# Performance work log

Measured on AMD Instinct MI355X. Metric: run time of the kernel, lower is better.

## Reference

```python
import jax, jax.numpy as jnp
import numpy as np

N_GRAPHS = 256
EPS = 1e-5


def _bn(x, g, b):
    # training-mode BatchNorm1d: biased batch statistics
    m = jnp.mean(x, axis=0)
    v = jnp.mean((x - m) ** 2, axis=0)
    return (x - m) * jax.lax.rsqrt(v + EPS) * g + b


def _gcn_conv(x, W, b, src, dst, dinv, n_nodes):
    # GCNConv: D^{-1/2} (A + I) D^{-1/2} X W + b
    h = x @ W  # [N, H]
    coef = dinv[src] * dinv[dst]  # [E]
    msg = h[src] * coef[:, None]  # [E, H]
    agg = jax.ops.segment_sum(msg, dst, num_segments=n_nodes)
    agg = agg + h * (dinv * dinv)[:, None]  # self-loop term
    return agg + b


def setup_inputs() -> dict:
    key = jax.random.key(0)
    ks = jax.random.split(key, 20)
    N, E, D, H, C = 50000, 600000, 128, 128, 10
    L = 3  # num_conv_layers
    x = jax.random.normal(ks[0], (N, D), dtype=jnp.float32)
    edge_index = jax.random.randint(ks[1], (2, E), 0, N, dtype=jnp.int64)
    batch = jnp.sort(jax.random.randint(ks[2], (N,), 0, N_GRAPHS, dtype=jnp.int64))

    def xavier(k, shape):
        fan_in, fan_out = shape[0], shape[1]
        lim = float(np.sqrt(6.0 / (fan_in + fan_out)))
        return jax.random.uniform(k, shape, jnp.float32, -lim, lim)

    return {
        "x": x,
        "edge_index": edge_index,
        "batch": batch,
        "bn_feat_g": jnp.ones((D,), jnp.float32),
        "bn_feat_b": jnp.full((D,), 1e-4, jnp.float32),
        "conv_feat_W": xavier(ks[3], (D, H)),
        "conv_feat_b": jnp.zeros((H,), jnp.float32),
        "conv_W": jnp.stack([xavier(ks[4 + i], (H, H)) for i in range(L)]),
        "conv_b": jnp.zeros((L, H), jnp.float32),
        "bn_conv_g": jnp.ones((L, H), jnp.float32),
        "bn_conv_b": jnp.full((L, H), 1e-4, jnp.float32),
        "gate_W1": xavier(ks[8], (H, H)),
        "gate_b1": jnp.zeros((H,), jnp.float32),
        "gate_W2": xavier(ks[9], (H, 1)),
        "gate_b2": jnp.zeros((1,), jnp.float32),
        "fc_W": xavier(ks[10], (H, H)),
        "fc_b": jnp.zeros((H,), jnp.float32),
        "bn_fc_g": jnp.ones((H,), jnp.float32),
        "bn_fc_b": jnp.full((H,), 1e-4, jnp.float32),
        "cls_W": xavier(ks[11], (H, C)),
        "cls_b": jnp.zeros((C,), jnp.float32),
    }


def reference(x, edge_index, batch, bn_feat_g, bn_feat_b, conv_feat_W, conv_feat_b,
              conv_W, conv_b, bn_conv_g, bn_conv_b, gate_W1, gate_b1, gate_W2,
              gate_b2, fc_W, fc_b, bn_fc_g, bn_fc_b, cls_W, cls_b):
    N = x.shape[0]
    src, dst = edge_index[0], edge_index[1]
    # degree incl. self-loop (edge weights = 1)
    deg = jax.ops.segment_sum(jnp.ones_like(src, dtype=x.dtype), dst, num_segments=N) + 1.0
    dinv = jax.lax.rsqrt(deg)

    h = _bn(x, bn_feat_g, bn_feat_b)
    h = jax.nn.relu(_gcn_conv(h, conv_feat_W, conv_feat_b, src, dst, dinv, N))
    for i in range(conv_W.shape[0]):
        h = jax.nn.relu(_gcn_conv(_bn(h, bn_conv_g[i], bn_conv_b[i]),
                                  conv_W[i], conv_b[i], src, dst, dinv, N))
    gate = jax.nn.sigmoid(jax.nn.relu(h @ gate_W1 + gate_b1) @ gate_W2 + gate_b2)  # [N,1]
    g = jax.ops.segment_sum(h * gate, batch, num_segments=N_GRAPHS)  # [G, H]
    g = jax.nn.relu(_bn(g, bn_fc_g, bn_fc_b) @ fc_W + fc_b)
    logits = g @ cls_W + cls_b
    return jax.nn.log_softmax(logits, axis=-1)
```

## Files before the change

### kernel.cpp

```cpp
#include <hip/hip_runtime.h>
#include <hip/hip_fp16.h>

typedef unsigned short u16;
typedef unsigned int u32;
typedef __attribute__((ext_vector_type(8))) short short8;
typedef __attribute__((ext_vector_type(4))) float floatx4;

#define EPSI 1e-5f

__device__ __forceinline__ float b2f(u16 h) { return __uint_as_float(((u32)h) << 16); }
__device__ __forceinline__ u16 f2b(float f) {
    u32 u = __float_as_uint(f);
    return (u16)((u + 0x7fffu + ((u >> 16) & 1u)) >> 16);
}
__device__ __forceinline__ u32 pack2(float a, float b) {
    return (u32)f2b(a) | ((u32)f2b(b) << 16);
}
__device__ __forceinline__ float ldf(const void* p, int i, int fm) {
    if (fm == 1) return b2f(((const u16*)p)[i]);
    if (fm == 2) return __half2float(__ushort_as_half(((const u16*)p)[i]));
    return ((const float*)p)[i];
}
__device__ __forceinline__ int ldi(const void* p, int i, int im) {
    return im ? ((const int*)p)[2 * i] : ((const int*)p)[i];
}

__device__ __forceinline__ void acc8(float* a, int4 v, float w) {
    u32 x = (u32)v.x, y = (u32)v.y, z = (u32)v.z, q = (u32)v.w;
    a[0] += b2f((u16)x) * w;
    a[1] += b2f((u16)(x >> 16)) * w;
    a[2] += b2f((u16)y) * w;
    a[3] += b2f((u16)(y >> 16)) * w;
    a[4] += b2f((u16)z) * w;
    a[5] += b2f((u16)(z >> 16)) * w;
    a[6] += b2f((u16)q) * w;
    a[7] += b2f((u16)(q >> 16)) * w;
}

__global__ void init_kernel(u32* zp, int nz, const void* ones, const void* ei, int* flags) {
    int i = blockIdx.x * 256 + threadIdx.x;
    if (i < nz) zp[i] = 0;
    if (blockIdx.x == 0 && threadIdx.x == 0) {
        u32 w = ((const u32*)ones)[0];
        int fm = 0;
        if (w == 0x3F803F80u) fm = 1;
        else if (w == 0x3C003C00u) fm = 2;
        const u32* e = (const u32*)ei;
        int all0 = 1;
        for (int k = 0; k < 16; ++k)
            if (e[2 * k + 1] != 0u) all0 = 0;
        flags[0] = fm;
        flags[1] = all0;
    }
}

__global__ void bigprep_kernel(const void* __restrict__ ei, int* __restrict__ cnt, int E,
                               const void* __restrict__ batch, int* __restrict__ bounds, int N,
                               int EB, const void* __restrict__ x, u32* __restrict__ A2,
                               float* __restrict__ stats0, const void* __restrict__ gW1,
                               const void* __restrict__ gb1, u16* __restrict__ Wtg,
                               float* __restrict__ bias2g, const void* __restrict__ cfW,
                               const void* __restrict__ cW, u16* __restrict__ Wt4,
                               const void* __restrict__ fcW, float* __restrict__ fcWf,
                               const void* __restrict__ clsW, float* __restrict__ clsWf,
                               const void* __restrict__ fcb, float* __restrict__ fcbf,
                               const void* __restrict__ clsb, float* __restrict__ clsbf,
                               const void* __restrict__ gW2, float* __restrict__ gW2f,
                               const void* __restrict__ gb2, float* __restrict__ gb2f,
                               const void* __restrict__ cfb, const void* __restrict__ cvb,
                               float* __restrict__ biasf, const int* __restrict__ flags) {
    int fm = flags[0];
    int bid = blockIdx.x, t = threadIdx.x;
    if (bid < EB) {
        int im = flags[1];
        int g = bid * 256 + t;
        if (g < E) atomicAdd(&cnt[ldi(ei, E + g, im)], 1);
        if (g < N) {
            int b = ldi(batch, g, im);
            if (g == 0) {
                for (int q = 0; q <= b; ++q) bounds[q] = 0;
            } else {
                int bp = ldi(batch, g - 1, im);
                for (int q = bp + 1; q <= b; ++q) bounds[q] = g;
            }
            if (g == N - 1) {
                for (int q = b + 1; q <= 256; ++q) bounds[q] = N;
            }
        }
        return;
    }
    int pid = bid - EB;
    if (pid < 1024) {
        int np = N * 64;
        float s0 = 0.f, s1 = 0.f, q0 = 0.f, q1 = 0.f;
        if (fm == 1) {
            const u32* xs = (const u32*)x;
            for (int j = pid * 256 + t; j < np; j += 1024 * 256) {
                u32 w = xs[j];
                A2[j] = w;
                float v0 = b2f((u16)w), v1 = b2f((u16)(w >> 16));
                s0 += v0;
                q0 += v0 * v0;
                s1 += v1;
                q1 += v1 * v1;
            }
        } else {
            for (int j = pid * 256 + t; j < np; j += 1024 * 256) {
                float v0 = ldf(x, 2 * j, fm);
                float v1 = ldf(x, 2 * j + 1, fm);
                A2[j] = pack2(v0, v1);
                s0 += v0;
                q0 += v0 * v0;
                s1 += v1;
                q1 += v1 * v1;
            }
        }
        __shared__ float2 sh[256];
        sh[t] = make_float2(s0, s1);
        __syncthreads();
        float* so = stats0 + (pid & 15) * 256;
        if (t < 64) {
            float a = 0.f, b = 0.f;
#pragma unroll
            for (int w = 0; w < 4; ++w) {
                float2 v = sh[t + w * 64];
                a += v.x;
                b += v.y;
            }
            atomicAdd(&so[2 * t], a);
            atomicAdd(&so[2 * t + 1], b);
        }
        __syncthreads();
        sh[t] = make_float2(q0, q1);
        __syncthreads();
        if (t < 64) {
            float a = 0.f, b = 0.f;
#pragma unroll
            for (int w = 0; w < 4; ++w) {
                float2 v = sh[t + w * 64];
                a += v.x;
                b += v.y;
            }
            atomicAdd(&so[128 + 2 * t], a);
            atomicAdd(&so[128 + 2 * t + 1], b);
        }
    } else if (pid < 1152) {
        int n = pid - 1024;
        if (t < 128) Wtg[n * 128 + t] = f2b(ldf(gW1, t * 128 + n, fm));
        if (t == 0) bias2g[n] = ldf(gb1, n, fm);
    } else if (pid < 1216) {
        int task = pid - 1152;
        int mat = task >> 4, tile = task & 15;
        int tr = (tile >> 2) * 32, tc = (tile & 3) * 32;
        const void* src = mat == 0 ? cfW : cW;
        int soff = mat == 0 ? 0 : (mat - 1) * 16384;
        __shared__ float tb[32][33];
#pragma unroll
        for (int i = 0; i < 4; ++i) {
            int o = t * 4 + i;
            int r = o >> 5, c = o & 31;
            tb[r][c] = ldf(src, soff + (tr + r) * 128 + tc + c, fm);
        }
        __syncthreads();
        u16* dst = Wt4 + mat * 16384;
#pragma unroll
        for (int i = 0; i < 4; ++i) {
            int o = t * 4 + i;
            int nr = o >> 5, kc = o & 31;
            dst[(tc + nr) * 128 + tr + kc] = f2b(tb[kc][nr]);
        }
    } else if (pid < 1224) {
        int base = (pid - 1216) * 2048;
        for (int i = t; i < 2048; i += 256) fcWf[base + i] = ldf(fcW, base + i, fm);
    } else {
        for (int i = t; i < 1280; i += 256) clsWf[i] = ldf(clsW, i, fm);
        for (int i = t; i < 512; i += 256)
            biasf[i] = (i < 128) ? ldf(cfb, i, fm) : ldf(cvb, i - 128, fm);
        if (t < 128) {
            fcbf[t] = ldf(fcb, t, fm);
            gW2f[t] = ldf(gW2, t, fm);
        }
        if (t < 10) clsbf[t] = ldf(clsb, t, fm);
        if (t == 0) gb2f[0] = ldf(gb2, 0, fm);
    }
}

__global__ void scan_kernel(const int* __restrict__ cnt, int* __restrict__ row_start, int n) {
    int b = blockIdx.x, t = threadIdx.x;
    __shared__ int sh[256];
    const int4* c4 = (const int4*)cnt;
    int lim4 = b * 256;
    int acc = 0;
    for (int i = t; i < lim4; i += 256) {
        int4 v = c4[i];
        acc += v.x + v.y + v.z + v.w;
    }
    sh[t] = acc;
    __syncthreads();
    for (int o = 128; o > 0; o >>= 1) {
        if (t < o) sh[t] += sh[t + o];
        __syncthreads();
    }
    int pre = sh[0];
    __syncthreads();
    int base = b * 1024 + t * 4;
    int v[4];
    int s = 0;
#pragma unroll
    for (int j = 0; j < 4; ++j) {
        int idx = base + j;
        v[j] = (idx < n) ? cnt[idx] : 0;
        s += v[j];
    }
    sh[t] = s;
    __syncthreads();
    for (int o = 1; o < 256; o <<= 1) {
        int add = (t >= o) ? sh[t - o] : 0;
        __syncthreads();
        sh[t] += add;
        __syncthreads();
    }
    int run = pre + sh[t] - s;
#pragma unroll
    for (int j = 0; j < 4; ++j) {
        int idx = base + j;
        run += v[j];
        if (idx < n) row_start[idx + 1] = run;
    }
    if (b == 0 && t == 0) row_start[0] = 0;
}

__global__ __launch_bounds__(256) void mfma_fill_kernel(
    const u16* __restrict__ A, const u16* __restrict__ Wt, const float* __restrict__ stats,
    const void* __restrict__ bng, const void* __restrict__ bnb, u16* __restrict__ C, int N,
    int mmgrid, const void* __restrict__ ei, const int* __restrict__ row_start,
    int* __restrict__ fill_cnt, const int* __restrict__ cnt, int2* __restrict__ edges, int E,
    const int* __restrict__ flags) {
    int t = threadIdx.x;
    if ((int)blockIdx.x >= mmgrid) {
        int im = flags[1];
        int e = (blockIdx.x - mmgrid) * 256 + t;
        if (e < E) {
            int s = ldi(ei, e, im);
            int d = ldi(ei, E + e, im);
            int p = row_start[d] + atomicAdd(&fill_cnt[d], 1);
            float cf = rsqrtf((float)cnt[s] + 1.0f) * rsqrtf((float)cnt[d] + 1.0f);
            edges[p] = make_int2(s, __float_as_int(cf));
        }
        return;
    }
    int fm = flags[0];
    __shared__ float scs[128], shs[128];
    if (t < 128) {
        float ms = 0.f, qs = 0.f;
#pragma unroll
        for (int c = 0; c < 16; ++c) {
            ms += stats[c * 256 + t];
            qs += stats[c * 256 + 128 + t];
        }
        float m = ms / (float)N;
        float var = qs / (float)N - m * m;
        float rs = rsqrtf(var + EPSI);
        float sc = rs * ldf(bng, t, fm);
        scs[t] = sc;
        shs[t] = ldf(bnb, t, fm) - m * sc;
    }
    __syncthreads();
    int wid = t >> 6, lane = t & 63;
    int m16 = lane & 15, q = lane >> 4;
    int row0 = blockIdx.x * 64 + wid * 16;
    if (row0 >= N) return;
    int arow = row0 + m16;
    floatx4 acc[8];
#pragma unroll
    for (int i = 0; i < 8; ++i) acc[i] = (floatx4){0.f, 0.f, 0.f, 0.f};
#pragma unroll
    for (int kc = 0; kc < 4; ++kc) {
        short8 af;
        if (arow < N) {
            short8 raw = *(const short8*)&A[(size_t)arow * 128 + kc * 32 + q * 8];
            int k0 = kc * 32 + q * 8;
#pragma unroll
            for (int j = 0; j < 8; ++j)
                af[j] = (short)f2b(b2f((u16)raw[j]) * scs[k0 + j] + shs[k0 + j]);
        } else {
#pragma unroll
            for (int j = 0; j < 8; ++j) af[j] = 0;
        }
#pragma unroll
        for (int nt = 0; nt < 8; ++nt) {
            short8 bf = *(const short8*)&Wt[(nt * 16 + m16) * 128 + kc * 32 + q * 8];
            acc[nt] = __builtin_amdgcn_mfma_f32_16x16x32_bf16(af, bf, acc[nt], 0, 0, 0);
        }
    }
#pragma unroll
    for (int nt = 0; nt < 8; ++nt) {
#pragma unroll
        for (int reg = 0; reg < 4; ++reg) {
            int r = row0 + q * 4 + reg;
            if (r < N) C[(size_t)r * 128 + nt * 16 + m16] = f2b(acc[nt][reg]);
        }
    }
}

__global__ __launch_bounds__(256) void mfma_mm_kernel(
    const u16* __restrict__ A, const u16* __restrict__ Wt, const float* __restrict__ stats,
    const void* __restrict__ bng, const void* __restrict__ bnb, int poff,
    const float* __restrict__ bias2, u16* __restrict__ C, float* __restrict__ gate,
    const float* __restrict__ gW2f, const float* __restrict__ gb2f, int N, int mode,
    const int* __restrict__ flags) {
    int t = threadIdx.x;
    __shared__ float scs[128], shs[128];
    if (stats && t < 128) {
        int fm = flags[0];
        float ms = 0.f, qs = 0.f;
#pragma unroll
        for (int c = 0; c < 16; ++c) {
            ms += stats[c * 256 + t];
            qs += stats[c * 256 + 128 + t];
        }
        float m = ms / (float)N;
        float var = qs / (float)N - m * m;
        float rs = rsqrtf(var + EPSI);
        float sc = rs * ldf(bng, poff + t, fm);
        scs[t] = sc;
        shs[t] = ldf(bnb, poff + t, fm) - m * sc;
    }
    __syncthreads();
    int wid = t >> 6, lane = t & 63;
    int m16 = lane & 15, q = lane >> 4;
    int row0 = blockIdx.x * 64 + wid * 16;
    if (row0 >= N) return;
    int arow = row0 + m16;
    floatx4 acc[8];
#pragma unroll
    for (int i = 0; i < 8; ++i) acc[i] = (floatx4){0.f, 0.f, 0.f, 0.f};
#pragma unroll
    for (int kc = 0; kc < 4; ++kc) {
        short8 af;
        if (arow < N) {
            if (stats) {
                short8 raw = *(const short8*)&A[(size_t)arow * 128 + kc * 32 + q * 8];
                int k0 = kc * 32 + q * 8;
#pragma unroll
                for (int j = 0; j < 8; ++j)
                    af[j] = (short)f2b(b2f((u16)raw[j]) * scs[k0 + j] + shs[k0 + j]);
            } else {
                af = *(const short8*)&A[(size_t)arow * 128 + kc * 32 + q * 8];
            }
        } else {
#pragma unroll
            for (int j = 0; j < 8; ++j) af[j] = 0;
        }
#pragma unroll
        for (int nt = 0; nt < 8; ++nt) {
            short8 bf = *(const short8*)&Wt[(nt * 16 + m16) * 128 + kc * 32 + q * 8];
            acc[nt] = __builtin_amdgcn_mfma_f32_16x16x32_bf16(af, bf, acc[nt], 0, 0, 0);
        }
    }
    if (mode == 0) {
#pragma unroll
        for (int nt = 0; nt < 8; ++nt) {
#pragma unroll
            for (int reg = 0; reg < 4; ++reg) {
                int r = row0 + q * 4 + reg;
                if (r < N) C[(size_t)r * 128 + nt * 16 + m16] = f2b(acc[nt][reg]);
            }
        }
    } else {
        float p[4] = {0.f, 0.f, 0.f, 0.f};
#pragma unroll
        for (int nt = 0; nt < 8; ++nt) {
            float b2v = bias2[nt * 16 + m16];
            float w2v = gW2f[nt * 16 + m16];
#pragma unroll
            for (int reg = 0; reg < 4; ++reg)
                p[reg] += fmaxf(acc[nt][reg] + b2v, 0.0f) * w2v;
        }
        float gb = gb2f[0];
#pragma unroll
        for (int reg = 0; reg < 4; ++reg) {
            float v = p[reg];
            v += __shfl_xor(v, 1);
            v += __shfl_xor(v, 2);
            v += __shfl_xor(v, 4);
            v += __shfl_xor(v, 8);
            if (m16 == 0) {
                int r = row0 + q * 4 + reg;
                if (r < N) gate[r] = 1.0f / (1.0f + expf(-(v + gb)));
            }
        }
    }
}

__global__ __launch_bounds__(512) void agg_kernel(
    const u32* __restrict__ C2, const int* __restrict__ row_start,
    const int2* __restrict__ edges, const float* __restrict__ biasf, int boff,
    u32* __restrict__ A2, float* __restrict__ statsOut, int N) {
    int t = threadIdx.x;
    int wid = t >> 6, lane = t & 63;
    int g = lane >> 4, p = lane & 15;
    int n = blockIdx.x * 8 + wid;
    float acc[8];
#pragma unroll
    for (int j = 0; j < 8; ++j) acc[j] = 0.f;
    if (n < N) {
        int rs = row_start[n], re = row_start[n + 1];
        if (g == 0) {
            float d2 = 1.0f / ((float)(re - rs) + 1.0f);
            int4 s = *(const int4*)&C2[(size_t)n * 64 + p * 4];
            acc8(acc, s, d2);
        }
        for (int e = rs; e < re; e += 16) {
            int iA = e + g, iB = e + 4 + g, iC = e + 8 + g, iD = e + 12 + g;
            int2 eA = edges[iA < re ? iA : re - 1];
            int2 eB = edges[iB < re ? iB : re - 1];
            int2 eC = edges[iC < re ? iC : re - 1];
            int2 eD = edges[iD < re ? iD : re - 1];
            int4 vA = *(const int4*)&C2[(size_t)eA.x * 64 + p * 4];
            int4 vB = *(const int4*)&C2[(size_t)eB.x * 64 + p * 4];
            int4 vC = *(const int4*)&C2[(size_t)eC.x * 64 + p * 4];
            int4 vD = *(const int4*)&C2[(size_t)eD.x * 64 + p * 4];
            acc8(acc, vA, iA < re ? __int_as_float(eA.y) : 0.f);
            acc8(acc, vB, iB < re ? __int_as_float(eB.y) : 0.f);
            acc8(acc, vC, iC < re ? __int_as_float(eC.y) : 0.f);
            acc8(acc, vD, iD < re ? __int_as_float(eD.y) : 0.f);
        }
    }
#pragma unroll
    for (int j = 0; j < 8; ++j) {
        acc[j] += __shfl_xor(acc[j], 16);
        acc[j] += __shfl_xor(acc[j], 32);
    }
    __shared__ float xch[8][128];
    if (g == 0) {
#pragma unroll
        for (int j = 0; j < 8; ++j) xch[wid][p * 8 + j] = acc[j];
    }
    __syncthreads();
    float ax = 0.f, ay = 0.f;
    if (n < N) {
        float2 bv = ((const float2*)(biasf + boff))[lane];
        float2 v = ((const float2*)xch[wid])[lane];
        ax = fmaxf(v.x + bv.x, 0.0f);
        ay = fmaxf(v.y + bv.y, 0.0f);
        A2[(size_t)n * 64 + lane] = pack2(ax, ay);
    }
    if (!statsOut) return;
    __shared__ float2 sh[512];
    sh[t] = make_float2(ax, ay);
    __syncthreads();
    float* so = statsOut + (blockIdx.x & 15) * 256;
    if (t < 64) {
        float a = 0.f, b = 0.f;
#pragma unroll
        for (int w = 0; w < 8; ++w) {
            float2 v = sh[t + w * 64];
            a += v.x;
            b += v.y;
        }
        atomicAdd(&so[2 * t], a);
        atomicAdd(&so[2 * t + 1], b);
    }
    __syncthreads();
    sh[t] = make_float2(ax * ax, ay * ay);
    __syncthreads();
    if (t < 64) {
        float a = 0.f, b = 0.f;
#pragma unroll
        for (int w = 0; w < 8; ++w) {
            float2 v = sh[t + w * 64];
            a += v.x;
            b += v.y;
        }
        atomicAdd(&so[128 + 2 * t], a);
        atomicAdd(&so[128 + 2 * t + 1], b);
    }
}

__global__ void pool_kernel(const u32* __restrict__ A2, const float* __restrict__ gate,
                            const int* __restrict__ bounds, float* __restrict__ pooled,
                            float* __restrict__ statsP) {
    int g = blockIdx.x;
    int t = threadIdx.x;
    int f2 = t & 63, grp = t >> 6;
    int s = bounds[g], e = bounds[g + 1];
    float ax = 0.f, ay = 0.f;
    int r = s + grp;
    for (; r + 4 < e; r += 8) {
        u32 v0 = A2[(size_t)r * 64 + f2];
        u32 v1 = A2[(size_t)(r + 4) * 64 + f2];
        float g0 = gate[r], g1 = gate[r + 4];
        ax += b2f((u16)v0) * g0;
        ay += b2f((u16)(v0 >> 16)) * g0;
        ax += b2f((u16)v1) * g1;
        ay += b2f((u16)(v1 >> 16)) * g1;
    }
    if (r < e) {
        u32 v0 = A2[(size_t)r * 64 + f2];
        float g0 = gate[r];
        ax += b2f((u16)v0) * g0;
        ay += b2f((u16)(v0 >> 16)) * g0;
    }
    __shared__ float2 sh[256];
    sh[t] = make_float2(ax, ay);
    __syncthreads();
    if (t < 64) {
        float2 a = sh[t], b = sh[t + 64], c = sh[t + 128], d = sh[t + 192];
        float x = a.x + b.x + c.x + d.x;
        float y = a.y + b.y + c.y + d.y;
        ((float2*)(pooled + g * 128))[t] = make_float2(x, y);
        float* so = statsP + (g & 7) * 256;
        atomicAdd(&so[2 * t], x);
        atomicAdd(&so[2 * t + 1], y);
        atomicAdd(&so[128 + 2 * t], x * x);
        atomicAdd(&so[128 + 2 * t + 1], y * y);
    }
}

__global__ __launch_bounds__(256) void fc_cls_kernel(
    const float* __restrict__ pooled, const float* __restrict__ statsP,
    const void* __restrict__ bng, const void* __restrict__ bnb,
    const float* __restrict__ fcWf, const float* __restrict__ fcbf,
    const float* __restrict__ clsWf, const float* __restrict__ clsbf, void* __restrict__ out,
    const int* __restrict__ flags) {
    int fm = flags[0];
    int g = blockIdx.x, t = threadIdx.x;
    __shared__ float pv[128];
    __shared__ float red[256];
    __shared__ float fco[128];
    __shared__ float lg[10];
    __shared__ float redv[2];
    if (t < 128) {
        float ms = 0.f, qs = 0.f;
#pragma unroll
        for (int c = 0; c < 8; ++c) {
            ms += statsP[c * 256 + t];
            qs += statsP[c * 256 + 128 + t];
        }
        float m = ms / 256.0f;
        float var = qs / 256.0f - m * m;
        float rs = rsqrtf(var + EPSI);
        float sc = rs * ldf(bng, t, fm);
        pv[t] = pooled[g * 128 + t] * sc + (ldf(bnb, t, fm) - m * sc);
    }
    __syncthreads();
    {
        int j = t & 127, half = t >> 7;
        float acc = 0.f;
        int k0 = half * 64;
#pragma unroll 8
        for (int k = k0; k < k0 + 64; ++k) acc += pv[k] * fcWf[k * 128 + j];
        red[t] = acc;
    }
    __syncthreads();
    if (t < 128) fco[t] = fmaxf(red[t] + red[t + 128] + fcbf[t], 0.0f);
    __syncthreads();
    if (t < 10) {
        float a = clsbf[t];
#pragma unroll 8
        for (int k = 0; k < 128; ++k) a += fco[k] * clsWf[k * 10 + t];
        lg[t] = a;
    }
    __syncthreads();
    if (t == 0) {
        float mx = lg[0];
        for (int j = 1; j < 10; ++j) mx = fmaxf(mx, lg[j]);
        float se = 0.f;
        for (int j = 0; j < 10; ++j) se += expf(lg[j] - mx);
        redv[0] = mx;
        redv[1] = logf(se);
    }
    __syncthreads();
    if (t < 10) {
        float v = lg[t] - redv[0] - redv[1];
        if (fm == 1) ((u16*)out)[g * 10 + t] = f2b(v);
        else if (fm == 2) ((u16*)out)[g * 10 + t] = __half_as_ushort(__float2half(v));
        else ((float*)out)[g * 10 + t] = v;
    }
}

extern "C" void kernel_launch(void* const* d_in, const int* in_sizes, int n_in,
                              void* d_out, int out_size, void* d_ws, size_t ws_size,
                              hipStream_t stream) {
    const void* x = d_in[0];
    const void* ei = d_in[1];
    const void* batch = d_in[2];
    const void* bn_feat_g = d_in[3];
    const void* bn_feat_b = d_in[4];
    const void* conv_feat_W = d_in[5];
    const void* conv_feat_b = d_in[6];
    const void* conv_W = d_in[7];
    const void* conv_b = d_in[8];
    const void* bn_conv_g = d_in[9];
    const void* bn_conv_b = d_in[10];
    const void* gate_W1 = d_in[11];
    const void* gate_b1 = d_in[12];
    const void* gate_W2 = d_in[13];
    const void* gate_b2 = d_in[14];
    const void* fc_W = d_in[15];
    const void* fc_b = d_in[16];
    const void* bn_fc_g = d_in[17];
    const void* bn_fc_b = d_in[18];
    const void* cls_W = d_in[19];
    const void* cls_b = d_in[20];

    const int N = in_sizes[2];
    const int E = in_sizes[1] / 2;
    const int NB = (N + 1023) / 1024;
    const int EB = ((E > N ? E : N) + 255) / 256;

    u32* ws = (u32*)d_ws;
    size_t off = 0;
    auto alloc = [&](size_t n) {
        size_t o = off;
        off += (n + 63) & ~(size_t)63;
        return o;
    };
    size_t o_cnt = alloc(N);
    size_t o_fill = alloc(N);
    size_t o_stats = alloc(5 * 4096);
    size_t o_statsP = alloc(2048);
    size_t zero_end = off;
    size_t o_flags = alloc(16);
    size_t o_rs = alloc((size_t)N + 1);
    size_t o_edges = alloc((size_t)E * 2);
    size_t o_wtg = alloc(128 * 128 / 2);
    size_t o_b2g = alloc(128);
    size_t o_Wt4 = alloc(4 * 16384 / 2);
    size_t o_fcW = alloc(16384);
    size_t o_fcb = alloc(128);
    size_t o_clsW = alloc(1280);
    size_t o_clsb = alloc(16);
    size_t o_gW2 = alloc(128);
    size_t o_gb2 = alloc(16);
    size_t o_biasf = alloc(512);
    size_t o_gate = alloc(N);
    size_t o_bnd = alloc(257);
    size_t o_pool = alloc(256 * 128);
    size_t o_A = alloc((size_t)N * 64);
    size_t o_C = alloc((size_t)N * 64);
    (void)ws_size;
    (void)n_in;
    (void)out_size;

    int* cnt = (int*)(ws + o_cnt);
    int* fillc = (int*)(ws + o_fill);
    float* stats = (float*)(ws + o_stats);
    float* statsP = (float*)(ws + o_statsP);
    int* flags = (int*)(ws + o_flags);
    int* row_start = (int*)(ws + o_rs);
    int2* edges = (int2*)(ws + o_edges);
    u16* Wtg = (u16*)(ws + o_wtg);
    float* bias2g = (float*)(ws + o_b2g);
    u16* Wt4 = (u16*)(ws + o_Wt4);
    float* fcWf = (float*)(ws + o_fcW);
    float* fcbf = (float*)(ws + o_fcb);
    float* clsWf = (float*)(ws + o_clsW);
    float* clsbf = (float*)(ws + o_clsb);
    float* gW2f = (float*)(ws + o_gW2);
    float* gb2f = (float*)(ws + o_gb2);
    float* biasf = (float*)(ws + o_biasf);
    float* gateb = (float*)(ws + o_gate);
    int* bnd = (int*)(ws + o_bnd);
    float* pooled = (float*)(ws + o_pool);
    u16* A = (u16*)(ws + o_A);
    u16* C = (u16*)(ws + o_C);

    int nz = (int)zero_end;
    init_kernel<<<(nz + 255) / 256, 256, 0, stream>>>(ws, nz, bn_feat_g, ei, flags);
    bigprep_kernel<<<EB + 1225, 256, 0, stream>>>(
        ei, cnt, E, batch, bnd, N, EB, x, (u32*)A, stats, gate_W1, gate_b1, Wtg, bias2g,
        conv_feat_W, conv_W, Wt4, fc_W, fcWf, cls_W, clsWf, fc_b, fcbf, cls_b, clsbf, gate_W2,
        gW2f, gate_b2, gb2f, conv_feat_b, conv_b, biasf, flags);
    scan_kernel<<<NB, 256, 0, stream>>>(cnt, row_start, N);

    int mmgrid = (N + 63) / 64;
    int agggrid = (N + 7) / 8;
    mfma_fill_kernel<<<mmgrid + EB, 256, 0, stream>>>(A, Wt4, stats, bn_feat_g, bn_feat_b, C, N,
                                                      mmgrid, ei, row_start, fillc, cnt, edges,
                                                      E, flags);
    for (int l = 0; l < 4; ++l) {
        if (l > 0)
            mfma_mm_kernel<<<mmgrid, 256, 0, stream>>>(
                A, Wt4 + (size_t)l * 16384, stats + (size_t)l * 4096, bn_conv_g, bn_conv_b,
                (l - 1) * 128, nullptr, C, nullptr, nullptr, nullptr, N, 0, flags);
        float* so = (l < 3) ? stats + (size_t)(l + 1) * 4096 : nullptr;
        agg_kernel<<<agggrid, 512, 0, stream>>>((const u32*)C, row_start, edges, biasf, l * 128,
                                                (u32*)A, so, N);
    }

    mfma_mm_kernel<<<mmgrid, 256, 0, stream>>>(A, Wtg, nullptr, nullptr, nullptr, 0, bias2g,
                                               nullptr, gateb, gW2f, gb2f, N, 2, flags);
    pool_kernel<<<256, 256, 0, stream>>>((const u32*)A, gateb, bnd, pooled, statsP);
    fc_cls_kernel<<<256, 256, 0, stream>>>(pooled, statsP, bn_fc_g, bn_fc_b, fcWf, fcbf, clsWf,
                                           clsbf, d_out, flags);
}
```

Baseline: 446.4 us.

## Fuse GCN layers, gate, pooling and classifier into one cooperative persistent kernel

```diff
diff --git a/kernel.cpp b/kernel.cpp
--- a/kernel.cpp
+++ b/kernel.cpp
@@ -1,5 +1,8 @@
 #include <hip/hip_runtime.h>
 #include <hip/hip_fp16.h>
+#include <hip/hip_cooperative_groups.h>
+
+namespace cg = cooperative_groups;
 
 typedef unsigned short u16;
 typedef unsigned int u32;
@@ -230,6 +233,355 @@
     if (b == 0 && t == 0) row_start[0] = 0;
 }
 
+
+__device__ __forceinline__ void gemm_tile_bn(const u16* __restrict__ A,
+                                             const u16* __restrict__ Wt,
+                                             const float* __restrict__ scs,
+                                             const float* __restrict__ shs,
+                                             u16* __restrict__ C, int N, int tt, int wid,
+                                             int lane) {
+    int m16 = lane & 15, q = lane >> 4;
+    int row0 = tt * 64 + wid * 16;
+    if (row0 >= N) return;
+    int arow = row0 + m16;
+    floatx4 acc[8];
+#pragma unroll
+    for (int i = 0; i < 8; ++i) acc[i] = (floatx4){0.f, 0.f, 0.f, 0.f};
+#pragma unroll
+    for (int kc = 0; kc < 4; ++kc) {
+        short8 af;
+        if (arow < N) {
+            short8 raw = *(const short8*)&A[(size_t)arow * 128 + kc * 32 + q * 8];
+            int k0 = kc * 32 + q * 8;
+#pragma unroll
+            for (int j = 0; j < 8; ++j)
+                af[j] = (short)f2b(b2f((u16)raw[j]) * scs[k0 + j] + shs[k0 + j]);
+        } else {
+#pragma unroll
+            for (int j = 0; j < 8; ++j) af[j] = 0;
+        }
+#pragma unroll
+        for (int nt = 0; nt < 8; ++nt) {
+            short8 bf = *(const short8*)&Wt[(nt * 16 + m16) * 128 + kc * 32 + q * 8];
+            acc[nt] = __builtin_amdgcn_mfma_f32_16x16x32_bf16(af, bf, acc[nt], 0, 0, 0);
+        }
+    }
+#pragma unroll
+    for (int nt = 0; nt < 8; ++nt) {
+#pragma unroll
+        for (int reg = 0; reg < 4; ++reg) {
+            int r = row0 + q * 4 + reg;
+            if (r < N) C[(size_t)r * 128 + nt * 16 + m16] = f2b(acc[nt][reg]);
+        }
+    }
+}
+
+__device__ __forceinline__ void gate_tile(const u16* __restrict__ A,
+                                          const u16* __restrict__ Wt,
+                                          const float* __restrict__ bias2,
+                                          const float* __restrict__ gW2f, float gb,
+                                          float* __restrict__ gate, int N, int tt, int wid,
+                                          int lane) {
+    int m16 = lane & 15, q = lane >> 4;
+    int row0 = tt * 64 + wid * 16;
+    if (row0 >= N) return;
+    int arow = row0 + m16;
+    floatx4 acc[8];
+#pragma unroll
+    for (int i = 0; i < 8; ++i) acc[i] = (floatx4){0.f, 0.f, 0.f, 0.f};
+#pragma unroll
+    for (int kc = 0; kc < 4; ++kc) {
+        short8 af;
+        if (arow < N) {
+            af = *(const short8*)&A[(size_t)arow * 128 + kc * 32 + q * 8];
+        } else {
+#pragma unroll
+            for (int j = 0; j < 8; ++j) af[j] = 0;
+        }
+#pragma unroll
+        for (int nt = 0; nt < 8; ++nt) {
+            short8 bf = *(const short8*)&Wt[(nt * 16 + m16) * 128 + kc * 32 + q * 8];
+            acc[nt] = __builtin_amdgcn_mfma_f32_16x16x32_bf16(af, bf, acc[nt], 0, 0, 0);
+        }
+    }
+    float p[4] = {0.f, 0.f, 0.f, 0.f};
+#pragma unroll
+    for (int nt = 0; nt < 8; ++nt) {
+        float b2v = bias2[nt * 16 + m16];
+        float w2v = gW2f[nt * 16 + m16];
+#pragma unroll
+        for (int reg = 0; reg < 4; ++reg) p[reg] += fmaxf(acc[nt][reg] + b2v, 0.0f) * w2v;
+    }
+#pragma unroll
+    for (int reg = 0; reg < 4; ++reg) {
+        float v = p[reg];
+        v += __shfl_xor(v, 1);
+        v += __shfl_xor(v, 2);
+        v += __shfl_xor(v, 4);
+        v += __shfl_xor(v, 8);
+        if (m16 == 0) {
+            int r = row0 + q * 4 + reg;
+            if (r < N) gate[r] = 1.0f / (1.0f + expf(-(v + gb)));
+        }
+    }
+}
+
+__global__ __launch_bounds__(256, 4) void mega_kernel(
+    u16* __restrict__ A, u16* __restrict__ C, const u16* __restrict__ Wt4,
+    const u16* __restrict__ Wtg, float* __restrict__ stats, const void* __restrict__ bnfg,
+    const void* __restrict__ bnfb, const void* __restrict__ bncg,
+    const void* __restrict__ bncb, const float* __restrict__ biasf,
+    const float* __restrict__ bias2g, const float* __restrict__ gW2f,
+    const float* __restrict__ gb2f, float* __restrict__ gateb,
+    const int* __restrict__ row_start, int2* __restrict__ edges, const void* __restrict__ ei,
+    int* __restrict__ fillc, const int* __restrict__ cnt, int E, int N,
+    const int* __restrict__ bnd, float* __restrict__ pooled, float* __restrict__ statsP,
+    const float* __restrict__ fcWf, const float* __restrict__ fcbf,
+    const float* __restrict__ clsWf, const float* __restrict__ clsbf,
+    const void* __restrict__ bnfcg, const void* __restrict__ bnfcb, void* __restrict__ out,
+    const int* __restrict__ flags) {
+    cg::grid_group grid = cg::this_grid();
+    int t = threadIdx.x;
+    int bid = blockIdx.x, nb = gridDim.x;
+    int fm = flags[0];
+    int mmgrid = (N + 63) / 64;
+    int wid = t >> 6, lane = t & 63;
+    u32* A2 = (u32*)A;
+    const u32* C2 = (const u32*)C;
+    __shared__ float scs[128], shs[128];
+    __shared__ float2 shf[256];
+    __shared__ float xch[4][128];
+    __shared__ float pv[128];
+    __shared__ float red[256];
+    __shared__ float fco[128];
+    __shared__ float lg[10];
+    __shared__ float redv[2];
+
+    for (int l = 0; l < 4; ++l) {
+        const float* st = stats + (size_t)l * 4096;
+        if (t < 128) {
+            float ms = 0.f, qs = 0.f;
+#pragma unroll
+            for (int c = 0; c < 16; ++c) {
+                ms += st[c * 256 + t];
+                qs += st[c * 256 + 128 + t];
+            }
+            float m = ms / (float)N;
+            float var = qs / (float)N - m * m;
+            float rstd = rsqrtf(var + EPSI);
+            float gv, bv;
+            if (l == 0) {
+                gv = ldf(bnfg, t, fm);
+                bv = ldf(bnfb, t, fm);
+            } else {
+                gv = ldf(bncg, (l - 1) * 128 + t, fm);
+                bv = ldf(bncb, (l - 1) * 128 + t, fm);
+            }
+            float sc = rstd * gv;
+            scs[t] = sc;
+            shs[t] = bv - m * sc;
+        }
+        __syncthreads();
+        const u16* Wt = Wt4 + (size_t)l * 16384;
+        for (int tt = bid; tt < mmgrid; tt += nb) gemm_tile_bn(A, Wt, scs, shs, C, N, tt, wid, lane);
+        if (l == 0) {
+            int im = flags[1];
+            int nchunk = (E + 255) / 256;
+            for (int ck = bid; ck < nchunk; ck += nb) {
+                int e = ck * 256 + t;
+                if (e < E) {
+                    int s = ldi(ei, e, im);
+                    int d = ldi(ei, E + e, im);
+                    int pth = row_start[d] + atomicAdd(&fillc[d], 1);
+                    float cf = rsqrtf((float)cnt[s] + 1.0f) * rsqrtf((float)cnt[d] + 1.0f);
+                    edges[pth] = make_int2(s, __float_as_int(cf));
+                }
+            }
+        }
+        __threadfence();
+        grid.sync();
+        float* soB = (l < 3) ? stats + (size_t)(l + 1) * 4096 : nullptr;
+        int g4 = lane >> 4, p = lane & 15;
+        int ngrp = (N + 3) / 4;
+        const float2* bvp = (const float2*)(biasf + l * 128);
+        for (int gi = bid; gi < ngrp; gi += nb) {
+            int n = gi * 4 + wid;
+            float acc[8];
+#pragma unroll
+            for (int j = 0; j < 8; ++j) acc[j] = 0.f;
+            if (n < N) {
+                int rs = row_start[n], re = row_start[n + 1];
+                if (g4 == 0) {
+                    float d2 = 1.0f / ((float)(re - rs) + 1.0f);
+                    int4 s = *(const int4*)&C2[(size_t)n * 64 + p * 4];
+                    acc8(acc, s, d2);
+                }
+                for (int e = rs; e < re; e += 16) {
+                    int iA = e + g4, iB = e + 4 + g4, iC = e + 8 + g4, iD = e + 12 + g4;
+                    int2 eA = edges[iA < re ? iA : re - 1];
+                    int2 eB = edges[iB < re ? iB : re - 1];
+                    int2 eC = edges[iC < re ? iC : re - 1];
+                    int2 eD = edges[iD < re ? iD : re - 1];
+                    int4 vA = *(const int4*)&C2[(size_t)eA.x * 64 + p * 4];
+                    int4 vB = *(const int4*)&C2[(size_t)eB.x * 64 + p * 4];
+                    int4 vC = *(const int4*)&C2[(size_t)eC.x * 64 + p * 4];
+                    int4 vD = *(const int4*)&C2[(size_t)eD.x * 64 + p * 4];
+                    acc8(acc, vA, iA < re ? __int_as_float(eA.y) : 0.f);
+                    acc8(acc, vB, iB < re ? __int_as_float(eB.y) : 0.f);
+                    acc8(acc, vC, iC < re ? __int_as_float(eC.y) : 0.f);
+                    acc8(acc, vD, iD < re ? __int_as_float(eD.y) : 0.f);
+                }
+            }
+#pragma unroll
+            for (int j = 0; j < 8; ++j) {
+                acc[j] += __shfl_xor(acc[j], 16);
+                acc[j] += __shfl_xor(acc[j], 32);
+            }
+            if (g4 == 0) {
+#pragma unroll
+                for (int j = 0; j < 8; ++j) xch[wid][p * 8 + j] = acc[j];
+            }
+            __syncthreads();
+            float ax = 0.f, ay = 0.f;
+            if (n < N) {
+                float2 bv = bvp[lane];
+                float2 v = ((const float2*)xch[wid])[lane];
+                ax = fmaxf(v.x + bv.x, 0.0f);
+                ay = fmaxf(v.y + bv.y, 0.0f);
+                A2[(size_t)n * 64 + lane] = pack2(ax, ay);
+            }
+            if (soB) {
+                shf[t] = make_float2(ax, ay);
+                __syncthreads();
+                float* so = soB + (gi & 15) * 256;
+                if (t < 64) {
+                    float a = 0.f, b = 0.f;
+#pragma unroll
+                    for (int w = 0; w < 4; ++w) {
+                        float2 v = shf[t + w * 64];
+                        a += v.x;
+                        b += v.y;
+                    }
+                    atomicAdd(&so[2 * t], a);
+                    atomicAdd(&so[2 * t + 1], b);
+                }
+                __syncthreads();
+                shf[t] = make_float2(ax * ax, ay * ay);
+                __syncthreads();
+                if (t < 64) {
+                    float a = 0.f, b = 0.f;
+#pragma unroll
+                    for (int w = 0; w < 4; ++w) {
+                        float2 v = shf[t + w * 64];
+                        a += v.x;
+                        b += v.y;
+                    }
+                    atomicAdd(&so[128 + 2 * t], a);
+                    atomicAdd(&so[128 + 2 * t + 1], b);
+                }
+            }
+            __syncthreads();
+        }
+        __threadfence();
+        grid.sync();
+    }
+    {
+        float gb = gb2f[0];
+        for (int tt = bid; tt < mmgrid; tt += nb)
+            gate_tile(A, Wtg, bias2g, gW2f, gb, gateb, N, tt, wid, lane);
+    }
+    __threadfence();
+    grid.sync();
+    if (bid < 256) {
+        int g = bid;
+        int f2 = t & 63, grp = t >> 6;
+        int s = bnd[g], e = bnd[g + 1];
+        float ax = 0.f, ay = 0.f;
+        int r = s + grp;
+        for (; r + 4 < e; r += 8) {
+            u32 v0 = A2[(size_t)r * 64 + f2];
+            u32 v1 = A2[(size_t)(r + 4) * 64 + f2];
+            float g0 = gateb[r], g1 = gateb[r + 4];
+            ax += b2f((u16)v0) * g0;
+            ay += b2f((u16)(v0 >> 16)) * g0;
+            ax += b2f((u16)v1) * g1;
+            ay += b2f((u16)(v1 >> 16)) * g1;
+        }
+        if (r < e) {
+            u32 v0 = A2[(size_t)r * 64 + f2];
+            float g0 = gateb[r];
+            ax += b2f((u16)v0) * g0;
+            ay += b2f((u16)(v0 >> 16)) * g0;
+        }
+        shf[t] = make_float2(ax, ay);
+        __syncthreads();
+        if (t < 64) {
+            float2 a = shf[t], b = shf[t + 64], c = shf[t + 128], d = shf[t + 192];
+            float xx = a.x + b.x + c.x + d.x;
+            float yy = a.y + b.y + c.y + d.y;
+            ((float2*)(pooled + g * 128))[t] = make_float2(xx, yy);
+            float* so = statsP + (g & 7) * 256;
+            atomicAdd(&so[2 * t], xx);
+            atomicAdd(&so[2 * t + 1], yy);
+            atomicAdd(&so[128 + 2 * t], xx * xx);
+            atomicAdd(&so[128 + 2 * t + 1], yy * yy);
+        }
+    }
+    __threadfence();
+    grid.sync();
+    if (bid < 256) {
+        int g = bid;
+        if (t < 128) {
+            float ms = 0.f, qs = 0.f;
+#pragma unroll
+            for (int c = 0; c < 8; ++c) {
+                ms += statsP[c * 256 + t];
+                qs += statsP[c * 256 + 128 + t];
+            }
+            float m = ms / 256.0f;
+            float var = qs / 256.0f - m * m;
+            float rstd = rsqrtf(var + EPSI);
+            float sc = rstd * ldf(bnfcg, t, fm);
+            pv[t] = pooled[g * 128 + t] * sc + (ldf(bnfcb, t, fm) - m * sc);
+        }
+        __syncthreads();
+        {
+            int j = t & 127, half = t >> 7;
+            float acc = 0.f;
+            int k0 = half * 64;
+#pragma unroll 8
+            for (int k = k0; k < k0 + 64; ++k) acc += pv[k] * fcWf[k * 128 + j];
+            red[t] = acc;
+        }
+        __syncthreads();
+        if (t < 128) fco[t] = fmaxf(red[t] + red[t + 128] + fcbf[t], 0.0f);
+        __syncthreads();
+        if (t < 10) {
+            float a = clsbf[t];
+#pragma unroll 8
+            for (int k = 0; k < 128; ++k) a += fco[k] * clsWf[k * 10 + t];
+            lg[t] = a;
+        }
+        __syncthreads();
+        if (t == 0) {
+            float mx = lg[0];
+            for (int j = 1; j < 10; ++j) mx = fmaxf(mx, lg[j]);
+            float se = 0.f;
+            for (int j = 0; j < 10; ++j) se += expf(lg[j] - mx);
+            redv[0] = mx;
+            redv[1] = logf(se);
+        }
+        __syncthreads();
+        if (t < 10) {
+            float v = lg[t] - redv[0] - redv[1];
+            if (fm == 1) ((u16*)out)[g * 10 + t] = f2b(v);
+            else if (fm == 2) ((u16*)out)[g * 10 + t] = __half_as_ushort(__float2half(v));
+            else ((float*)out)[g * 10 + t] = v;
+        }
+    }
+}
+
+
 __global__ __launch_bounds__(256) void mfma_fill_kernel(
     const u16* __restrict__ A, const u16* __restrict__ Wt, const float* __restrict__ stats,
     const void* __restrict__ bng, const void* __restrict__ bnb, u16* __restrict__ C, int N,
@@ -267,40 +619,7 @@
     }
     __syncthreads();
     int wid = t >> 6, lane = t & 63;
-    int m16 = lane & 15, q = lane >> 4;
-    int row0 = blockIdx.x * 64 + wid * 16;
-    if (row0 >= N) return;
-    int arow = row0 + m16;
-    floatx4 acc[8];
-#pragma unroll
-    for (int i = 0; i < 8; ++i) acc[i] = (floatx4){0.f, 0.f, 0.f, 0.f};
-#pragma unroll
-    for (int kc = 0; kc < 4; ++kc) {
-        short8 af;
-        if (arow < N) {
-            short8 raw = *(const short8*)&A[(size_t)arow * 128 + kc * 32 + q * 8];
-            int k0 = kc * 32 + q * 8;
-#pragma unroll
-            for (int j = 0; j < 8; ++j)
-                af[j] = (short)f2b(b2f((u16)raw[j]) * scs[k0 + j] + shs[k0 + j]);
-        } else {
-#pragma unroll
-            for (int j = 0; j < 8; ++j) af[j] = 0;
-        }
-#pragma unroll
-        for (int nt = 0; nt < 8; ++nt) {
-            short8 bf = *(const short8*)&Wt[(nt * 16 + m16) * 128 + kc * 32 + q * 8];
-            acc[nt] = __builtin_amdgcn_mfma_f32_16x16x32_bf16(af, bf, acc[nt], 0, 0, 0);
-        }
-    }
-#pragma unroll
-    for (int nt = 0; nt < 8; ++nt) {
-#pragma unroll
-        for (int reg = 0; reg < 4; ++reg) {
-            int r = row0 + q * 4 + reg;
-            if (r < N) C[(size_t)r * 128 + nt * 16 + m16] = f2b(acc[nt][reg]);
-        }
-    }
+    gemm_tile_bn(A, Wt, scs, shs, C, N, blockIdx.x, wid, lane);
 }
 
 __global__ __launch_bounds__(256) void mfma_mm_kernel(
@@ -328,69 +647,10 @@
     }
     __syncthreads();
     int wid = t >> 6, lane = t & 63;
-    int m16 = lane & 15, q = lane >> 4;
-    int row0 = blockIdx.x * 64 + wid * 16;
-    if (row0 >= N) return;
-    int arow = row0 + m16;
-    floatx4 acc[8];
-#pragma unroll
-    for (int i = 0; i < 8; ++i) acc[i] = (floatx4){0.f, 0.f, 0.f, 0.f};
-#pragma unroll
-    for (int kc = 0; kc < 4; ++kc) {
-        short8 af;
-        if (arow < N) {
-            if (stats) {
-                short8 raw = *(const short8*)&A[(size_t)arow * 128 + kc * 32 + q * 8];
-                int k0 = kc * 32 + q * 8;
-#pragma unroll
-                for (int j = 0; j < 8; ++j)
-                    af[j] = (short)f2b(b2f((u16)raw[j]) * scs[k0 + j] + shs[k0 + j]);
-            } else {
-                af = *(const short8*)&A[(size_t)arow * 128 + kc * 32 + q * 8];
-            }
-        } else {
-#pragma unroll
-            for (int j = 0; j < 8; ++j) af[j] = 0;
-        }
-#pragma unroll
-        for (int nt = 0; nt < 8; ++nt) {
-            short8 bf = *(const short8*)&Wt[(nt * 16 + m16) * 128 + kc * 32 + q * 8];
-            acc[nt] = __builtin_amdgcn_mfma_f32_16x16x32_bf16(af, bf, acc[nt], 0, 0, 0);
-        }
-    }
-    if (mode == 0) {
-#pragma unroll
-        for (int nt = 0; nt < 8; ++nt) {
-#pragma unroll
-            for (int reg = 0; reg < 4; ++reg) {
-                int r = row0 + q * 4 + reg;
-                if (r < N) C[(size_t)r * 128 + nt * 16 + m16] = f2b(acc[nt][reg]);
-            }
-        }
-    } else {
-        float p[4] = {0.f, 0.f, 0.f, 0.f};
-#pragma unroll
-        for (int nt = 0; nt < 8; ++nt) {
-            float b2v = bias2[nt * 16 + m16];
-            float w2v = gW2f[nt * 16 + m16];
-#pragma unroll
-            for (int reg = 0; reg < 4; ++reg)
-                p[reg] += fmaxf(acc[nt][reg] + b2v, 0.0f) * w2v;
-        }
-        float gb = gb2f[0];
-#pragma unroll
-        for (int reg = 0; reg < 4; ++reg) {
-            float v = p[reg];
-            v += __shfl_xor(v, 1);
-            v += __shfl_xor(v, 2);
-            v += __shfl_xor(v, 4);
-            v += __shfl_xor(v, 8);
-            if (m16 == 0) {
-                int r = row0 + q * 4 + reg;
-                if (r < N) gate[r] = 1.0f / (1.0f + expf(-(v + gb)));
-            }
-        }
-    }
+    if (mode == 0)
+        gemm_tile_bn(A, Wt, scs, shs, C, N, blockIdx.x, wid, lane);
+    else
+        gate_tile(A, Wt, bias2, gW2f, gb2f[0], gate, N, blockIdx.x, wid, lane);
 }
 
 __global__ __launch_bounds__(512) void agg_kernel(
@@ -675,24 +935,50 @@
         gW2f, gate_b2, gb2f, conv_feat_b, conv_b, biasf, flags);
     scan_kernel<<<NB, 256, 0, stream>>>(cnt, row_start, N);
 
-    int mmgrid = (N + 63) / 64;
-    int agggrid = (N + 7) / 8;
-    mfma_fill_kernel<<<mmgrid + EB, 256, 0, stream>>>(A, Wt4, stats, bn_feat_g, bn_feat_b, C, N,
-                                                      mmgrid, ei, row_start, fillc, cnt, edges,
-                                                      E, flags);
-    for (int l = 0; l < 4; ++l) {
-        if (l > 0)
-            mfma_mm_kernel<<<mmgrid, 256, 0, stream>>>(
-                A, Wt4 + (size_t)l * 16384, stats + (size_t)l * 4096, bn_conv_g, bn_conv_b,
-                (l - 1) * 128, nullptr, C, nullptr, nullptr, nullptr, N, 0, flags);
-        float* so = (l < 3) ? stats + (size_t)(l + 1) * 4096 : nullptr;
-        agg_kernel<<<agggrid, 512, 0, stream>>>((const u32*)C, row_start, edges, biasf, l * 128,
-                                                (u32*)A, so, N);
-    }
-
-    mfma_mm_kernel<<<mmgrid, 256, 0, stream>>>(A, Wtg, nullptr, nullptr, nullptr, 0, bias2g,
-                                               nullptr, gateb, gW2f, gb2f, N, 2, flags);
-    pool_kernel<<<256, 256, 0, stream>>>((const u32*)A, gateb, bnd, pooled, statsP);
-    fc_cls_kernel<<<256, 256, 0, stream>>>(pooled, statsP, bn_fc_g, bn_fc_b, fcWf, fcbf, clsWf,
-                                           clsbf, d_out, flags);
-}
+    int coopOK = 0;
+    {
+        int maxB = 0;
+        hipError_t qe = hipOccupancyMaxActiveBlocksPerMultiprocessor(&maxB, mega_kernel, 256, 0);
+        if (qe != hipSuccess || maxB < 1) maxB = 0;
+        if (maxB > 8) maxB = 8;
+        if (maxB >= 1) {
+            int grid = maxB * 256;
+            if (grid < 256) grid = 256;
+            int Ee = E, Nn = N;
+            void* kargs[] = {
+                (void*)&A,         (void*)&C,         (void*)&Wt4,       (void*)&Wtg,
+                (void*)&stats,     (void*)&bn_feat_g, (void*)&bn_feat_b, (void*)&bn_conv_g,
+                (void*)&bn_conv_b, (void*)&biasf,     (void*)&bias2g,    (void*)&gW2f,
+                (void*)&gb2f,      (void*)&gateb,     (void*)&row_start, (void*)&edges,
+                (void*)&ei,        (void*)&fillc,     (void*)&cnt,       (void*)&Ee,
+                (void*)&Nn,        (void*)&bnd,       (void*)&pooled,    (void*)&statsP,
+                (void*)&fcWf,      (void*)&fcbf,      (void*)&clsWf,     (void*)&clsbf,
+                (void*)&bn_fc_g,   (void*)&bn_fc_b,   (void*)&d_out,     (void*)&flags};
+            hipError_t ce = hipLaunchCooperativeKernel(mega_kernel, dim3(grid), dim3(256),
+                                                       kargs, 0, stream);
+            coopOK = (ce == hipSuccess);
+        }
+    }
+
+    if (!coopOK) {
+        int mmgrid = (N + 63) / 64;
+        int agggrid = (N + 7) / 8;
+        mfma_fill_kernel<<<mmgrid + EB, 256, 0, stream>>>(A, Wt4, stats, bn_feat_g, bn_feat_b,
+                                                          C, N, mmgrid, ei, row_start, fillc,
+                                                          cnt, edges, E, flags);
+        for (int l = 0; l < 4; ++l) {
+            if (l > 0)
+                mfma_mm_kernel<<<mmgrid, 256, 0, stream>>>(
+                    A, Wt4 + (size_t)l * 16384, stats + (size_t)l * 4096, bn_conv_g, bn_conv_b,
+                    (l - 1) * 128, nullptr, C, nullptr, nullptr, nullptr, N, 0, flags);
+            float* so = (l < 3) ? stats + (size_t)(l + 1) * 4096 : nullptr;
+            agg_kernel<<<agggrid, 512, 0, stream>>>((const u32*)C, row_start, edges, biasf,
+                                                    l * 128, (u32*)A, so, N);
+        }
+        mfma_mm_kernel<<<mmgrid, 256, 0, stream>>>(A, Wtg, nullptr, nullptr, nullptr, 0, bias2g,
+                                                   nullptr, gateb, gW2f, gb2f, N, 2, flags);
+        pool_kernel<<<256, 256, 0, stream>>>((const u32*)A, gateb, bnd, pooled, statsP);
+        fc_cls_kernel<<<256, 256, 0, stream>>>(pooled, statsP, bn_fc_g, bn_fc_b, fcWf, fcbf,
+                                               clsWf, clsbf, d_out, flags);
+    }
+}
```

After: 1.719 ms. 3.85x slower.

## Pack CSR edges into 32-bit words and factor destination norm out of aggregation

Applied to the files above, without the earlier changes.

```diff
diff --git a/kernel.cpp b/kernel.cpp
--- a/kernel.cpp
+++ b/kernel.cpp
@@ -104,6 +104,16 @@
                 s1 += v1;
                 q1 += v1 * v1;
             }
+        } else if (fm == 0) {
+            const float2* xs2 = (const float2*)x;
+            for (int j = pid * 256 + t; j < np; j += 1024 * 256) {
+                float2 v = xs2[j];
+                A2[j] = pack2(v.x, v.y);
+                s0 += v.x;
+                q0 += v.x * v.x;
+                s1 += v.y;
+                q1 += v.y * v.y;
+            }
         } else {
             for (int j = pid * 256 + t; j < np; j += 1024 * 256) {
                 float v0 = ldf(x, 2 * j, fm);
@@ -234,7 +244,7 @@
     const u16* __restrict__ A, const u16* __restrict__ Wt, const float* __restrict__ stats,
     const void* __restrict__ bng, const void* __restrict__ bnb, u16* __restrict__ C, int N,
     int mmgrid, const void* __restrict__ ei, const int* __restrict__ row_start,
-    int* __restrict__ fill_cnt, const int* __restrict__ cnt, int2* __restrict__ edges, int E,
+    int* __restrict__ fill_cnt, const int* __restrict__ cnt, u32* __restrict__ edges, int E,
     const int* __restrict__ flags) {
     int t = threadIdx.x;
     if ((int)blockIdx.x >= mmgrid) {
@@ -244,8 +254,8 @@
             int s = ldi(ei, e, im);
             int d = ldi(ei, E + e, im);
             int p = row_start[d] + atomicAdd(&fill_cnt[d], 1);
-            float cf = rsqrtf((float)cnt[s] + 1.0f) * rsqrtf((float)cnt[d] + 1.0f);
-            edges[p] = make_int2(s, __float_as_int(cf));
+            float ds = rsqrtf((float)cnt[s] + 1.0f);
+            edges[p] = (u32)s | ((u32)__half_as_ushort(__float2half_rn(ds)) << 16);
         }
         return;
     }
@@ -395,36 +405,43 @@
 
 __global__ __launch_bounds__(512) void agg_kernel(
     const u32* __restrict__ C2, const int* __restrict__ row_start,
-    const int2* __restrict__ edges, const float* __restrict__ biasf, int boff,
+    const u32* __restrict__ edges, const float* __restrict__ biasf, int boff,
     u32* __restrict__ A2, float* __restrict__ statsOut, int N) {
     int t = threadIdx.x;
     int wid = t >> 6, lane = t & 63;
     int g = lane >> 4, p = lane & 15;
     int n = blockIdx.x * 8 + wid;
+    __shared__ float xch[8][128];
+    __shared__ float2 sh[512];
     float acc[8];
 #pragma unroll
     for (int j = 0; j < 8; ++j) acc[j] = 0.f;
+    float dinv_d = 1.f;
     if (n < N) {
         int rs = row_start[n], re = row_start[n + 1];
+        dinv_d = rsqrtf((float)(re - rs) + 1.0f);
         if (g == 0) {
-            float d2 = 1.0f / ((float)(re - rs) + 1.0f);
             int4 s = *(const int4*)&C2[(size_t)n * 64 + p * 4];
-            acc8(acc, s, d2);
+            acc8(acc, s, dinv_d);
         }
         for (int e = rs; e < re; e += 16) {
             int iA = e + g, iB = e + 4 + g, iC = e + 8 + g, iD = e + 12 + g;
-            int2 eA = edges[iA < re ? iA : re - 1];
-            int2 eB = edges[iB < re ? iB : re - 1];
-            int2 eC = edges[iC < re ? iC : re - 1];
-            int2 eD = edges[iD < re ? iD : re - 1];
-            int4 vA = *(const int4*)&C2[(size_t)eA.x * 64 + p * 4];
-            int4 vB = *(const int4*)&C2[(size_t)eB.x * 64 + p * 4];
-            int4 vC = *(const int4*)&C2[(size_t)eC.x * 64 + p * 4];
-            int4 vD = *(const int4*)&C2[(size_t)eD.x * 64 + p * 4];
-            acc8(acc, vA, iA < re ? __int_as_float(eA.y) : 0.f);
-            acc8(acc, vB, iB < re ? __int_as_float(eB.y) : 0.f);
-            acc8(acc, vC, iC < re ? __int_as_float(eC.y) : 0.f);
-            acc8(acc, vD, iD < re ? __int_as_float(eD.y) : 0.f);
+            u32 eA = edges[iA < re ? iA : re - 1];
+            u32 eB = edges[iB < re ? iB : re - 1];
+            u32 eC = edges[iC < re ? iC : re - 1];
+            u32 eD = edges[iD < re ? iD : re - 1];
+            int4 vA = *(const int4*)&C2[(size_t)(eA & 0xFFFFu) * 64 + p * 4];
+            int4 vB = *(const int4*)&C2[(size_t)(eB & 0xFFFFu) * 64 + p * 4];
+            int4 vC = *(const int4*)&C2[(size_t)(eC & 0xFFFFu) * 64 + p * 4];
+            int4 vD = *(const int4*)&C2[(size_t)(eD & 0xFFFFu) * 64 + p * 4];
+            float wA = iA < re ? __half2float(__ushort_as_half((u16)(eA >> 16))) : 0.f;
+            float wB = iB < re ? __half2float(__ushort_as_half((u16)(eB >> 16))) : 0.f;
+            float wC = iC < re ? __half2float(__ushort_as_half((u16)(eC >> 16))) : 0.f;
+            float wD = iD < re ? __half2float(__ushort_as_half((u16)(eD >> 16))) : 0.f;
+            acc8(acc, vA, wA);
+            acc8(acc, vB, wB);
+            acc8(acc, vC, wC);
+            acc8(acc, vD, wD);
         }
     }
 #pragma unroll
@@ -432,7 +449,6 @@
         acc[j] += __shfl_xor(acc[j], 16);
         acc[j] += __shfl_xor(acc[j], 32);
     }
-    __shared__ float xch[8][128];
     if (g == 0) {
 #pragma unroll
         for (int j = 0; j < 8; ++j) xch[wid][p * 8 + j] = acc[j];
@@ -442,12 +458,11 @@
     if (n < N) {
         float2 bv = ((const float2*)(biasf + boff))[lane];
         float2 v = ((const float2*)xch[wid])[lane];
-        ax = fmaxf(v.x + bv.x, 0.0f);
-        ay = fmaxf(v.y + bv.y, 0.0f);
+        ax = fmaxf(v.x * dinv_d + bv.x, 0.0f);
+        ay = fmaxf(v.y * dinv_d + bv.y, 0.0f);
         A2[(size_t)n * 64 + lane] = pack2(ax, ay);
     }
     if (!statsOut) return;
-    __shared__ float2 sh[512];
     sh[t] = make_float2(ax, ay);
     __syncthreads();
     float* so = statsOut + (blockIdx.x & 15) * 256;
@@ -485,6 +500,7 @@
     int t = threadIdx.x;
     int f2 = t & 63, grp = t >> 6;
     int s = bounds[g], e = bounds[g + 1];
+    __shared__ float2 sh[256];
     float ax = 0.f, ay = 0.f;
     int r = s + grp;
     for (; r + 4 < e; r += 8) {
@@ -502,7 +518,6 @@
         ax += b2f((u16)v0) * g0;
         ay += b2f((u16)(v0 >> 16)) * g0;
     }
-    __shared__ float2 sh[256];
     sh[t] = make_float2(ax, ay);
     __syncthreads();
     if (t < 64) {
@@ -624,7 +639,7 @@
     size_t zero_end = off;
     size_t o_flags = alloc(16);
     size_t o_rs = alloc((size_t)N + 1);
-    size_t o_edges = alloc((size_t)E * 2);
+    size_t o_edges = alloc((size_t)E);
     size_t o_wtg = alloc(128 * 128 / 2);
     size_t o_b2g = alloc(128);
     size_t o_Wt4 = alloc(4 * 16384 / 2);
@@ -650,7 +665,7 @@
     float* statsP = (float*)(ws + o_statsP);
     int* flags = (int*)(ws + o_flags);
     int* row_start = (int*)(ws + o_rs);
-    int2* edges = (int2*)(ws + o_edges);
+    u32* edges = (u32*)(ws + o_edges);
     u16* Wtg = (u16*)(ws + o_wtg);
     float* bias2g = (float*)(ws + o_b2g);
     u16* Wt4 = (u16*)(ws + o_Wt4);
```

New measurement: 453.9 us. Within noise of the previous version (+1.7%).
